# Kernel optimization log

Measured on AMD Instinct MI355X. Metric: run time of the kernel, lower is better.

## Reference

```python
import jax, jax.numpy as jnp
import numpy as np

N_NODES = 50000
N_EDGES = 800000
N_GLOBALS = 64
DX, DE, DU = 128, 32, 32
HID, OUT = 128, 128
EPS = 1e-5


def _mlp(x, W1, b1, W2, b2, g, b):
    # Linear -> ReLU -> Linear -> ReLU (activate_final) -> LayerNorm (normalize)
    h = jax.nn.relu(x @ W1 + b1)
    h = jax.nn.relu(h @ W2 + b2)
    mu = jnp.mean(h, axis=-1, keepdims=True)
    var = jnp.var(h, axis=-1, keepdims=True)
    return g * (h - mu) * jax.lax.rsqrt(var + EPS) + b


def _mlp_params(key, d_in):
    k1, k2 = jax.random.split(key)
    W1 = jax.random.normal(k1, (d_in, HID), jnp.float32) / np.sqrt(d_in)
    b1 = jnp.zeros((HID,), jnp.float32)
    W2 = jax.random.normal(k2, (HID, OUT), jnp.float32) / np.sqrt(HID)
    b2 = jnp.zeros((OUT,), jnp.float32)
    g = jnp.ones((OUT,), jnp.float32)
    b = jnp.zeros((OUT,), jnp.float32)
    return W1, b1, W2, b2, g, b


def setup_inputs() -> dict:
    key = jax.random.key(0)
    ks = jax.random.split(key, 8)
    x = jax.random.normal(ks[0], (N_NODES, DX), jnp.float32)
    e = jax.random.normal(ks[1], (N_EDGES, DE), jnp.float32)
    u = jax.random.normal(ks[2], (N_GLOBALS, DU), jnp.float32)
    edge_index = jax.random.randint(ks[3], (2, N_EDGES), 0, N_NODES, jnp.int64 if jax.config.jax_enable_x64 else jnp.int32)
    batch = jnp.sort(jax.random.randint(ks[4], (N_NODES,), 0, N_GLOBALS))
    # edge MLP in: e(32) + recv(128) + send(128) + u(32) = 320
    eW1, eb1, eW2, eb2, eg, ebt = _mlp_params(ks[5], DE + DX + DX + DU)
    # node MLP in: x(128) + edge_aggr(128) + u(32) = 288
    nW1, nb1, nW2, nb2, ng, nbt = _mlp_params(ks[6], DX + OUT + DU)
    # global MLP in: u(32) + node_aggr(128) + edge_aggr(128) = 288
    gW1, gb1, gW2, gb2, gg, gbt = _mlp_params(ks[7], DU + OUT + OUT)
    return dict(x=x, e=e, u=u, edge_index=edge_index, batch=batch,
                eW1=eW1, eb1=eb1, eW2=eW2, eb2=eb2, eg=eg, ebt=ebt,
                nW1=nW1, nb1=nb1, nW2=nW2, nb2=nb2, ng=ng, nbt=nbt,
                gW1=gW1, gb1=gb1, gW2=gW2, gb2=gb2, gg=gg, gbt=gbt)


def reference(x, e, u, edge_index, batch,
              eW1, eb1, eW2, eb2, eg, ebt,
              nW1, nb1, nW2, nb2, ng, nbt,
              gW1, gb1, gW2, gb2, gg, gbt):
    row, col = edge_index[0], edge_index[1]
    edge_batch = batch[row]  # graph id per edge

    # --- EdgeModel: concat(edge, receiver, sender, global->edges) -> MLP ---
    edge_in = jnp.concatenate([e, x[col], x[row], u[edge_batch]], axis=1)
    e2 = _mlp(edge_in, eW1, eb1, eW2, eb2, eg, ebt)  # [N_EDGES, OUT]

    # --- NodeModel: concat(node, edges->node via receiver, global->nodes) -> MLP ---
    edge_to_node = jax.ops.segment_sum(e2, col, num_segments=N_NODES)
    node_in = jnp.concatenate([x, edge_to_node, u[batch]], axis=1)
    x2 = _mlp(node_in, nW1, nb1, nW2, nb2, ng, nbt)  # [N_NODES, OUT]

    # --- GlobalModel: concat(global, nodes->global, edges->global) -> MLP ---
    node_to_glob = jax.ops.segment_sum(x2, batch, num_segments=N_GLOBALS)
    edge_to_glob = jax.ops.segment_sum(e2, edge_batch, num_segments=N_GLOBALS)
    glob_in = jnp.concatenate([u, node_to_glob, edge_to_glob], axis=1)
    u2 = _mlp(glob_in, gW1, gb1, gW2, gb2, gg, gbt)  # [N_GLOBALS, OUT]

    return x2, e2, u2
```

## Files before the change

### kernel.cpp

```cpp
#include <hip/hip_runtime.h>
#include <hip/hip_bf16.h>

typedef __attribute__((ext_vector_type(8))) short bf16x8;
typedef __attribute__((ext_vector_type(4))) float f32x4;

#define EPSV 1e-5f
#define NN 50000
#define NE 800000
#define NG 64
#define SEGB 1000
#define MFMA16(a, b, c) __builtin_amdgcn_mfma_f32_16x16x32_bf16(a, b, c, 0, 0, 0)

__device__ __forceinline__ unsigned short f2bf(float f) {
  union { float f; unsigned u; } v; v.f = f;
  unsigned r = v.u + 0x7FFFu + ((v.u >> 16) & 1u);
  return (unsigned short)(r >> 16);
}
__device__ __forceinline__ float bf2f(unsigned short h) {
  union { unsigned u; float f; } v; v.u = ((unsigned)h) << 16;
  return v.f;
}
__device__ __forceinline__ float bflo(unsigned u) {
  union { unsigned x; float f; } v; v.x = u << 16; return v.f;
}
__device__ __forceinline__ float bfhi(unsigned u) {
  union { unsigned x; float f; } v; v.x = u & 0xffff0000u; return v.f;
}


__global__ __launch_bounds__(256) void cvt_vec_kernel(
    const float* __restrict__ x, unsigned short* __restrict__ xb) {
  const int NX4 = (NN * 128) / 4;
  for (int idx = blockIdx.x * 256 + threadIdx.x; idx < NX4;
       idx += gridDim.x * 256) {
    float4 v = ((const float4*)x)[idx];
    ushort4 o;
    o.x = f2bf(v.x); o.y = f2bf(v.y); o.z = f2bf(v.z); o.w = f2bf(v.w);
    ((ushort4*)xb)[idx] = o;
  }
}

__global__ __launch_bounds__(256) void cvt_small_kernel(
    const float* __restrict__ u,
    const float* __restrict__ eW1, const float* __restrict__ eW2,
    const float* __restrict__ nW1, const float* __restrict__ nW2,
    unsigned short* __restrict__ ub,
    unsigned short* __restrict__ W1eT, unsigned short* __restrict__ WpqT,
    unsigned short* __restrict__ eW2T,
    unsigned short* __restrict__ nW1T, unsigned short* __restrict__ nW2T,
    float* __restrict__ Rg) {
  int i = blockIdx.x * 256 + threadIdx.x;
  const int R0 = NG * 32;
  const int R1 = R0 + 128 * 32;
  const int R2 = R1 + 256 * 128;
  const int R3 = R2 + 128 * 128;
  const int R4 = R3 + 128 * 320;
  const int R5 = R4 + 128 * 128;
  const int R6 = R5 + NG * 128;
  if (i < R0) {
    ub[i] = f2bf(u[i]);
  } else if (i < R1) {
    int j = i - R0; int n = j >> 5, k = j & 31;
    W1eT[j] = f2bf(eW1[k * 128 + n]);
  } else if (i < R2) {
    int j = i - R1; int n = j >> 7, k = j & 127;
    WpqT[j] = (n < 128) ? f2bf(eW1[(32 + k) * 128 + n])
                        : f2bf(eW1[(160 + k) * 128 + (n - 128)]);
  } else if (i < R3) {
    int j = i - R2; int n = j >> 7, k = j & 127;
    eW2T[j] = f2bf(eW2[k * 128 + n]);
  } else if (i < R4) {
    int j = i - R3; int n = j / 320, k = j % 320;
    nW1T[j] = (k < 288) ? f2bf(nW1[k * 128 + n]) : (unsigned short)0;
  } else if (i < R5) {
    int j = i - R4; int n = j >> 7, k = j & 127;
    nW2T[j] = f2bf(nW2[k * 128 + n]);
  } else if (i < R6) {
    int j = i - R5; int g = j >> 7, n = j & 127;
    float s = 0.f;
#pragma unroll
    for (int k = 0; k < 32; ++k) s += u[g * 32 + k] * eW1[(288 + k) * 128 + n];
    Rg[j] = s;
  }
}

__global__ __launch_bounds__(256, 2) void pq_kernel(
    const unsigned short* __restrict__ xb,
    const unsigned short* __restrict__ WpqT,
    unsigned short* __restrict__ PQ) {
  __shared__ __align__(16) unsigned short Asm[64][136];
  __shared__ __align__(16) unsigned short Bsm[256][72];
  const int tid = threadIdx.x;
  {
    const int r = tid >> 2, q = tid & 3;
    const int grow = blockIdx.x * 64 + r;
    const uint4 zero = {0u, 0u, 0u, 0u};
    if (grow < NN) {
      const uint4* xs = (const uint4*)(xb + (size_t)grow * 128 + q * 32);
#pragma unroll
      for (int k = 0; k < 4; ++k) *(uint4*)&Asm[r][q * 32 + k * 8] = xs[k];
    } else {
#pragma unroll
      for (int k = 0; k < 4; ++k) *(uint4*)&Asm[r][q * 32 + k * 8] = zero;
    }
  }
  const int w = tid >> 6, lane = tid & 63;
  const int l15 = lane & 15, lg = lane >> 4;
  f32x4 acc[16];
#pragma unroll
  for (int ni = 0; ni < 16; ++ni) acc[ni] = f32x4{0.f, 0.f, 0.f, 0.f};
  for (int kc = 0; kc < 2; ++kc) {
    {
      const uint4* src = (const uint4*)(WpqT + (size_t)tid * 128 + kc * 64);
#pragma unroll
      for (int k = 0; k < 8; ++k) *(uint4*)&Bsm[tid][k * 8] = src[k];
    }
    __syncthreads();
    bf16x8 a0 = *(bf16x8*)&Asm[w * 16 + l15][kc * 64 + lg * 8];
    bf16x8 a1 = *(bf16x8*)&Asm[w * 16 + l15][kc * 64 + 32 + lg * 8];
#pragma unroll
    for (int ni = 0; ni < 16; ++ni) {
      bf16x8 b0 = *(bf16x8*)&Bsm[ni * 16 + l15][lg * 8];
      bf16x8 b1 = *(bf16x8*)&Bsm[ni * 16 + l15][32 + lg * 8];
      acc[ni] = MFMA16(a0, b0, acc[ni]);
      acc[ni] = MFMA16(a1, b1, acc[ni]);
    }
    __syncthreads();
  }
  unsigned short (*Cl)[264] = (unsigned short(*)[264])&Bsm[0][0];
#pragma unroll
  for (int ni = 0; ni < 16; ++ni)
#pragma unroll
    for (int reg = 0; reg < 4; ++reg)
      Cl[w * 16 + lg * 4 + reg][l15 + ni * 16] = f2bf(acc[ni][reg]);
  __syncthreads();
  {
    const int r = tid >> 2, q = tid & 3;
    const int grow = blockIdx.x * 64 + r;
    if (grow < NN) {
#pragma unroll
      for (int k = 0; k < 8; ++k)
        *(uint4*)(PQ + (size_t)grow * 256 + q * 64 + k * 8) =
            *(uint4*)&Cl[r][q * 64 + k * 8];
    }
  }
}


__global__ __launch_bounds__(256) void pre_kernel(
    const int* __restrict__ rowIdx, const int* __restrict__ colIdx,
    int* __restrict__ cnt_r, int* __restrict__ cnt_s) {
  int i = blockIdx.x * 256 + threadIdx.x;
  if (i < NE) {
    atomicAdd(&cnt_r[colIdx[i]], 1);
    atomicAdd(&cnt_s[rowIdx[i]], 1);
  }
}

__global__ __launch_bounds__(1024) void scan2_kernel(
    const int* __restrict__ cnt_r, int* __restrict__ offs_r, int* __restrict__ cur_r,
    const int* __restrict__ cnt_s, int* __restrict__ offs_s, int* __restrict__ cur_s) {
  __shared__ int sums[1024];
  const int* cnt = blockIdx.x ? cnt_s : cnt_r;
  int* offs = blockIdx.x ? offs_s : offs_r;
  int* cur  = blockIdx.x ? cur_s : cur_r;
  const int t = threadIdx.x;
  const int base = t * 49;
  int s = 0;
  for (int j = 0; j < 49; ++j) {
    int idx = base + j;
    if (idx < NN) s += cnt[idx];
  }
  sums[t] = s;
  __syncthreads();
  for (int off = 1; off < 1024; off <<= 1) {
    int add = (t >= off) ? sums[t - off] : 0;
    __syncthreads();
    sums[t] += add;
    __syncthreads();
  }
  int run = (t == 0) ? 0 : sums[t - 1];
  for (int j = 0; j < 49; ++j) {
    int idx = base + j;
    if (idx < NN) {
      offs[idx] = run; cur[idx] = run;
      run += cnt[idx];
    }
  }
}

__global__ __launch_bounds__(256) void fill_both_kernel(
    const int* __restrict__ rowIdx, const int* __restrict__ colIdx,
    const int* __restrict__ batch,
    int* __restrict__ cur_r, int* __restrict__ cur_s,
    int* __restrict__ eidlist_r, int* __restrict__ eidlist_s,
    int* __restrict__ gs) {
  int i = blockIdx.x * 256 + threadIdx.x;
  if (i < NE) {
    const int c = colIdx[i];
    const int p = atomicAdd(&cur_r[c], 1);
    eidlist_r[p] = i;
    const int r = rowIdx[i];
    const int p2 = atomicAdd(&cur_s[r], 1);
    eidlist_s[p2] = i;
    gs[p2] = batch[r];
  }
}

__global__ __launch_bounds__(256, 3) void edge_kernel(
    const float* __restrict__ ef,
    const unsigned short* __restrict__ PQ,
    const float* __restrict__ Rg,
    const int* __restrict__ rowI, const int* __restrict__ colI,
    const int* __restrict__ batch,
    const unsigned short* __restrict__ W1eT,
    const unsigned short* __restrict__ W2T,
    const float* __restrict__ b1, const float* __restrict__ b2,
    const float* __restrict__ gam, const float* __restrict__ bet,
    float* __restrict__ outE, unsigned short* __restrict__ e2b) {
  __shared__ __align__(16) char U[27648];
  __shared__ __align__(16) unsigned short Hsm[64][136];
  __shared__ float cb1[128], cb2[128], cg[128], cbt[128];
  unsigned short (*B1e)[40] = (unsigned short(*)[40])U;
  unsigned short (*Ssm)[136] = (unsigned short(*)[136])(U + 10240);
  unsigned short (*Bsm)[72] = (unsigned short(*)[72])U;

  const int tid = threadIdx.x;
  const int base = blockIdx.x * 64;
  if (tid < 128) {
    cb1[tid] = b1[tid]; cb2[tid] = b2[tid];
    cg[tid] = gam[tid]; cbt[tid] = bet[tid];
    const uint4* s = (const uint4*)(W1eT + tid * 32);
#pragma unroll
    for (int k = 0; k < 4; ++k) *(uint4*)&B1e[tid][k * 8] = s[k];
  }

  {
    const int r = tid >> 2, q = tid & 3;
    const int grow = base + r;
    const int rcv = colI[grow];
    const int snd = rowI[grow];
    const int g = batch[snd];
    const unsigned short* pp = PQ + (size_t)rcv * 256 + q * 32;
    const unsigned short* qq = PQ + (size_t)snd * 256 + 128 + q * 32;
    const float* rr = Rg + g * 128 + q * 32;
#pragma unroll
    for (int k = 0; k < 8; ++k) {
      ushort4 pv = *(const ushort4*)(pp + k * 4);
      ushort4 qv = *(const ushort4*)(qq + k * 4);
      float4 rv = *(const float4*)(rr + k * 4);
      ushort4 o;
      o.x = f2bf(bf2f(pv.x) + bf2f(qv.x) + rv.x);
      o.y = f2bf(bf2f(pv.y) + bf2f(qv.y) + rv.y);
      o.z = f2bf(bf2f(pv.z) + bf2f(qv.z) + rv.z);
      o.w = f2bf(bf2f(pv.w) + bf2f(qv.w) + rv.w);
      *(ushort4*)&Ssm[r][q * 32 + k * 4] = o;
    }
  }
  __syncthreads();

  const int w = tid >> 6, lane = tid & 63;
  const int l15 = lane & 15, lg = lane >> 4;

  f32x4 acc[8];
#pragma unroll
  for (int ni = 0; ni < 8; ++ni) acc[ni] = f32x4{0.f, 0.f, 0.f, 0.f};
  {
    const int arow = base + w * 16 + l15;
    const float* ep = ef + (size_t)arow * 32 + lg * 8;
    float4 v0 = *(const float4*)ep;
    float4 v1 = *(const float4*)(ep + 4);
    bf16x8 a;
    a[0] = (short)f2bf(v0.x); a[1] = (short)f2bf(v0.y);
    a[2] = (short)f2bf(v0.z); a[3] = (short)f2bf(v0.w);
    a[4] = (short)f2bf(v1.x); a[5] = (short)f2bf(v1.y);
    a[6] = (short)f2bf(v1.z); a[7] = (short)f2bf(v1.w);
#pragma unroll
    for (int ni = 0; ni < 8; ++ni) {
      bf16x8 b0 = *(bf16x8*)&B1e[ni * 16 + l15][lg * 8];
      acc[ni] = MFMA16(a, b0, acc[ni]);
    }
  }

#pragma unroll
  for (int ni = 0; ni < 8; ++ni) {
    const int ncol = l15 + ni * 16;
    const float bias = cb1[ncol];
#pragma unroll
    for (int reg = 0; reg < 4; ++reg) {
      const int mrow = w * 16 + lg * 4 + reg;
      const float sv = bf2f(Ssm[mrow][ncol]);
      Hsm[mrow][ncol] = f2bf(fmaxf(acc[ni][reg] + sv + bias, 0.f));
    }
  }
  __syncthreads();

  f32x4 acc2[8];
#pragma unroll
  for (int ni = 0; ni < 8; ++ni) acc2[ni] = f32x4{0.f, 0.f, 0.f, 0.f};
  for (int kc = 0; kc < 2; ++kc) {
    {
      const int n = tid >> 1, half = tid & 1;
      const uint4* src = (const uint4*)(W2T + (size_t)n * 128 + kc * 64 + half * 32);
#pragma unroll
      for (int k = 0; k < 4; ++k)
        *(uint4*)&Bsm[n][half * 32 + k * 8] = src[k];
    }
    __syncthreads();
    bf16x8 a0 = *(bf16x8*)&Hsm[w * 16 + l15][kc * 64 + lg * 8];
    bf16x8 a1 = *(bf16x8*)&Hsm[w * 16 + l15][kc * 64 + 32 + lg * 8];
#pragma unroll
    for (int ni = 0; ni < 8; ++ni) {
      bf16x8 b0 = *(bf16x8*)&Bsm[ni * 16 + l15][lg * 8];
      bf16x8 b1 = *(bf16x8*)&Bsm[ni * 16 + l15][32 + lg * 8];
      acc2[ni] = MFMA16(a0, b0, acc2[ni]);
      acc2[ni] = MFMA16(a1, b1, acc2[ni]);
    }
    __syncthreads();
  }

  float hv[8][4];
  float sreg[4] = {0.f, 0.f, 0.f, 0.f}, ssreg[4] = {0.f, 0.f, 0.f, 0.f};
#pragma unroll
  for (int ni = 0; ni < 8; ++ni) {
    const int ncol = l15 + ni * 16;
    const float bias = cb2[ncol];
#pragma unroll
    for (int reg = 0; reg < 4; ++reg) {
      const float h = fmaxf(acc2[ni][reg] + bias, 0.f);
      hv[ni][reg] = h;
      sreg[reg] += h; ssreg[reg] += h * h;
    }
  }
#pragma unroll
  for (int reg = 0; reg < 4; ++reg) {
    float s = sreg[reg], ss = ssreg[reg];
#pragma unroll
    for (int off = 1; off < 16; off <<= 1) {
      s += __shfl_xor(s, off, 64);
      ss += __shfl_xor(ss, off, 64);
    }
    sreg[reg] = s; ssreg[reg] = ss;
  }
#pragma unroll
  for (int reg = 0; reg < 4; ++reg) {
    const int mrow = w * 16 + lg * 4 + reg;
    const int grow = base + mrow;
    const float mu = sreg[reg] * (1.f / 128.f);
    const float var = ssreg[reg] * (1.f / 128.f) - mu * mu;
    const float rstd = rsqrtf(var + EPSV);
#pragma unroll
    for (int ni = 0; ni < 8; ++ni) {
      const int ncol = l15 + ni * 16;
      const float y = cg[ncol] * (hv[ni][reg] - mu) * rstd + cbt[ncol];
      outE[(size_t)grow * 128 + ncol] = y;
      if (e2b) Hsm[mrow][ncol] = f2bf(y);
    }
  }
  if (e2b) {
    __syncthreads();
    const int r = tid >> 2, q = tid & 3;
#pragma unroll
    for (int k = 0; k < 4; ++k)
      *(uint4*)(e2b + (size_t)(base + r) * 128 + q * 32 + k * 8) =
          *(uint4*)&Hsm[r][q * 32 + k * 8];
  }
}

template <int BF>
__global__ __launch_bounds__(256, 2) void post_kernel(
    const float* __restrict__ outE, const unsigned short* __restrict__ e2b,
    const int* __restrict__ eidl_s, const int* __restrict__ gsA,
    float* __restrict__ e2g,
    const unsigned short* __restrict__ xb,
    const unsigned short* __restrict__ ub,
    const int* __restrict__ batch,
    const int* __restrict__ offs, const int* __restrict__ cnt,
    const int* __restrict__ eidlist,
    const unsigned short* __restrict__ W1T,
    const unsigned short* __restrict__ W2T,
    const float* __restrict__ b1, const float* __restrict__ b2,
    const float* __restrict__ gam, const float* __restrict__ bet,
    float* __restrict__ outX, float* __restrict__ n2g) {
  __shared__ __align__(16) char U[50176];
  __shared__ __align__(16) unsigned short Bsm[128][72];
  __shared__ float cb1[128], cb2[128], cg[128], cbt[128];

  const int tid = threadIdx.x;

  if (blockIdx.x < SEGB) {
    const int c4 = (tid & 31) * 4;
    const int sub = tid >> 5;
    const int start = blockIdx.x * 800;
    int gcur = gsA[start + sub];
    float4 acc = {0.f, 0.f, 0.f, 0.f};
    for (int it = 0; it < 25; ++it) {
      const int pbase = start + sub + it * 32;
      int eid[4], g[4];
#pragma unroll
      for (int j = 0; j < 4; ++j) {
        eid[j] = eidl_s[pbase + j * 8];
        g[j]   = gsA[pbase + j * 8];
      }
      float4 v[4];
      if (BF) {
#pragma unroll
        for (int j = 0; j < 4; ++j) {
          ushort4 h = *(const ushort4*)(e2b + (size_t)eid[j] * 128 + c4);
          v[j] = float4{bf2f(h.x), bf2f(h.y), bf2f(h.z), bf2f(h.w)};
        }
      } else {
#pragma unroll
        for (int j = 0; j < 4; ++j)
          v[j] = *(const float4*)(outE + (size_t)eid[j] * 128 + c4);
      }
#pragma unroll
      for (int j = 0; j < 4; ++j) {
        if (g[j] != gcur) {
          atomicAdd(&e2g[gcur * 128 + c4],     acc.x);
          atomicAdd(&e2g[gcur * 128 + c4 + 1], acc.y);
          atomicAdd(&e2g[gcur * 128 + c4 + 2], acc.z);
          atomicAdd(&e2g[gcur * 128 + c4 + 3], acc.w);
          gcur = g[j]; acc = float4{0.f, 0.f, 0.f, 0.f};
        }
        acc.x += v[j].x; acc.y += v[j].y; acc.z += v[j].z; acc.w += v[j].w;
      }
    }
    atomicAdd(&e2g[gcur * 128 + c4],     acc.x);
    atomicAdd(&e2g[gcur * 128 + c4 + 1], acc.y);
    atomicAdd(&e2g[gcur * 128 + c4 + 2], acc.z);
    atomicAdd(&e2g[gcur * 128 + c4 + 3], acc.w);
    return;
  }

  const int bx = blockIdx.x - SEGB;
  unsigned short (*Asm)[328] = (unsigned short(*)[328])U;
  unsigned short (*Hsm)[136] = (unsigned short(*)[136])U;
  float* bins = (float*)(U + 17408);

  if (tid < 128) {
    cb1[tid] = b1[tid]; cb2[tid] = b2[tid];
    cg[tid] = gam[tid]; cbt[tid] = bet[tid];
  }

  {
    const int r = tid >> 2, q = tid & 3;
    const int grow = bx * 64 + r;
    const bool valid = grow < NN;
    const uint4 zero = {0u, 0u, 0u, 0u};
    if (valid) {
      const uint4* xs = (const uint4*)(xb + (size_t)grow * 128 + q * 32);
#pragma unroll
      for (int k = 0; k < 4; ++k) *(uint4*)&Asm[r][q * 32 + k * 8] = xs[k];
    } else {
#pragma unroll
      for (int k = 0; k < 4; ++k) *(uint4*)&Asm[r][q * 32 + k * 8] = zero;
    }
    float4 a[8];
#pragma unroll
    for (int k = 0; k < 8; ++k) a[k] = float4{0.f, 0.f, 0.f, 0.f};
    if (valid) {
      const int start = offs[grow];
      const int deg = cnt[grow];
      int j = 0;
      for (; j + 2 <= deg; j += 2) {
        const int e0 = eidlist[start + j], e1 = eidlist[start + j + 1];
        if (BF) {
          const uint4* s0 = (const uint4*)(e2b + (size_t)e0 * 128 + q * 32);
          const uint4* s1 = (const uint4*)(e2b + (size_t)e1 * 128 + q * 32);
#pragma unroll
          for (int k = 0; k < 4; ++k) {
            uint4 v0 = s0[k], v1 = s1[k];
            a[2 * k].x     += bflo(v0.x) + bflo(v1.x);
            a[2 * k].y     += bfhi(v0.x) + bfhi(v1.x);
            a[2 * k].z     += bflo(v0.y) + bflo(v1.y);
            a[2 * k].w     += bfhi(v0.y) + bfhi(v1.y);
            a[2 * k + 1].x += bflo(v0.z) + bflo(v1.z);
            a[2 * k + 1].y += bfhi(v0.z) + bfhi(v1.z);
            a[2 * k + 1].z += bflo(v0.w) + bflo(v1.w);
            a[2 * k + 1].w += bfhi(v0.w) + bfhi(v1.w);
          }
        } else {
          const float4* s0 = (const float4*)(outE + (size_t)e0 * 128 + q * 32);
          const float4* s1 = (const float4*)(outE + (size_t)e1 * 128 + q * 32);
#pragma unroll
          for (int k = 0; k < 8; ++k) {
            float4 v0 = s0[k], v1 = s1[k];
            a[k].x += v0.x + v1.x; a[k].y += v0.y + v1.y;
            a[k].z += v0.z + v1.z; a[k].w += v0.w + v1.w;
          }
        }
      }
      if (j < deg) {
        const int e0 = eidlist[start + j];
        if (BF) {
          const uint4* s0 = (const uint4*)(e2b + (size_t)e0 * 128 + q * 32);
#pragma unroll
          for (int k = 0; k < 4; ++k) {
            uint4 v0 = s0[k];
            a[2 * k].x     += bflo(v0.x);
            a[2 * k].y     += bfhi(v0.x);
            a[2 * k].z     += bflo(v0.y);
            a[2 * k].w     += bfhi(v0.y);
            a[2 * k + 1].x += bflo(v0.z);
            a[2 * k + 1].y += bfhi(v0.z);
            a[2 * k + 1].z += bflo(v0.w);
            a[2 * k + 1].w += bfhi(v0.w);
          }
        } else {
          const float4* s0 = (const float4*)(outE + (size_t)e0 * 128 + q * 32);
#pragma unroll
          for (int k = 0; k < 8; ++k) {
            float4 v0 = s0[k];
            a[k].x += v0.x; a[k].y += v0.y; a[k].z += v0.z; a[k].w += v0.w;
          }
        }
      }
    }
#pragma unroll
    for (int k = 0; k < 8; ++k) {
      ushort4 o;
      o.x = f2bf(a[k].x); o.y = f2bf(a[k].y);
      o.z = f2bf(a[k].z); o.w = f2bf(a[k].w);
      *(ushort4*)&Asm[r][128 + q * 32 + k * 4] = o;
    }
    const int g = valid ? batch[grow] : 0;
    uint4 uv = valid ? *(const uint4*)(ub + g * 32 + q * 8) : zero;
    *(uint4*)&Asm[r][256 + q * 8] = uv;
    *(uint4*)&Asm[r][288 + q * 8] = zero;
  }

  const int w = tid >> 6;
  const int lane = tid & 63;
  const int l15 = lane & 15, lg = lane >> 4;

  f32x4 acc[8];
#pragma unroll
  for (int ni = 0; ni < 8; ++ni) acc[ni] = f32x4{0.f, 0.f, 0.f, 0.f};

  for (int kc = 0; kc < 5; ++kc) {
    {
      const int n = tid >> 1, half = tid & 1;
      const uint4* src = (const uint4*)(W1T + (size_t)n * 320 + kc * 64 + half * 32);
#pragma unroll
      for (int k = 0; k < 4; ++k)
        *(uint4*)&Bsm[n][half * 32 + k * 8] = src[k];
    }
    __syncthreads();
    bf16x8 a0 = *(bf16x8*)&Asm[w * 16 + l15][kc * 64 + lg * 8];
    bf16x8 a1 = *(bf16x8*)&Asm[w * 16 + l15][kc * 64 + 32 + lg * 8];
#pragma unroll
    for (int ni = 0; ni < 8; ++ni) {
      bf16x8 bb0 = *(bf16x8*)&Bsm[ni * 16 + l15][lg * 8];
      bf16x8 bb1 = *(bf16x8*)&Bsm[ni * 16 + l15][32 + lg * 8];
      acc[ni] = MFMA16(a0, bb0, acc[ni]);
      acc[ni] = MFMA16(a1, bb1, acc[ni]);
    }
    __syncthreads();
  }

#pragma unroll
  for (int ni = 0; ni < 8; ++ni) {
    const int ncol = l15 + ni * 16;
    const float bias = cb1[ncol];
#pragma unroll
    for (int reg = 0; reg < 4; ++reg) {
      const int mrow = w * 16 + lg * 4 + reg;
      Hsm[mrow][ncol] = f2bf(fmaxf(acc[ni][reg] + bias, 0.f));
    }
  }
  for (int i = tid; i < NG * 128; i += 256) bins[i] = 0.f;

  f32x4 acc2[8];
#pragma unroll
  for (int ni = 0; ni < 8; ++ni) acc2[ni] = f32x4{0.f, 0.f, 0.f, 0.f};
  for (int kc = 0; kc < 2; ++kc) {
    {
      const int n = tid >> 1, half = tid & 1;
      const uint4* src = (const uint4*)(W2T + (size_t)n * 128 + kc * 64 + half * 32);
#pragma unroll
      for (int k = 0; k < 4; ++k)
        *(uint4*)&Bsm[n][half * 32 + k * 8] = src[k];
    }
    __syncthreads();
    bf16x8 a0 = *(bf16x8*)&Hsm[w * 16 + l15][kc * 64 + lg * 8];
    bf16x8 a1 = *(bf16x8*)&Hsm[w * 16 + l15][kc * 64 + 32 + lg * 8];
#pragma unroll
    for (int ni = 0; ni < 8; ++ni) {
      bf16x8 bb0 = *(bf16x8*)&Bsm[ni * 16 + l15][lg * 8];
      bf16x8 bb1 = *(bf16x8*)&Bsm[ni * 16 + l15][32 + lg * 8];
      acc2[ni] = MFMA16(a0, bb0, acc2[ni]);
      acc2[ni] = MFMA16(a1, bb1, acc2[ni]);
    }
    __syncthreads();
  }

  float hv[8][4];
  float sreg[4] = {0.f, 0.f, 0.f, 0.f}, ssreg[4] = {0.f, 0.f, 0.f, 0.f};
#pragma unroll
  for (int ni = 0; ni < 8; ++ni) {
    const int ncol = l15 + ni * 16;
    const float bias = cb2[ncol];
#pragma unroll
    for (int reg = 0; reg < 4; ++reg) {
      const float h = fmaxf(acc2[ni][reg] + bias, 0.f);
      hv[ni][reg] = h;
      sreg[reg] += h; ssreg[reg] += h * h;
    }
  }
#pragma unroll
  for (int reg = 0; reg < 4; ++reg) {
    float s = sreg[reg], ss = ssreg[reg];
#pragma unroll
    for (int off = 1; off < 16; off <<= 1) {
      s += __shfl_xor(s, off, 64);
      ss += __shfl_xor(ss, off, 64);
    }
    sreg[reg] = s; ssreg[reg] = ss;
  }
#pragma unroll
  for (int reg = 0; reg < 4; ++reg) {
    const int mrow = w * 16 + lg * 4 + reg;
    const int grow = bx * 64 + mrow;
    if (grow >= NN) continue;
    const float mu = sreg[reg] * (1.f / 128.f);
    const float var = ssreg[reg] * (1.f / 128.f) - mu * mu;
    const float rstd = rsqrtf(var + EPSV);
    const int g = batch[grow];
#pragma unroll
    for (int ni = 0; ni < 8; ++ni) {
      const int ncol = l15 + ni * 16;
      const float y = cg[ncol] * (hv[ni][reg] - mu) * rstd + cbt[ncol];
      outX[(size_t)grow * 128 + ncol] = y;
      atomicAdd(&bins[g * 128 + ncol], y);
    }
  }
  __syncthreads();
  const int first = bx * 64;
  const int last = min(first + 63, NN - 1);
  const int gmin = batch[first], gmax = batch[last];
  const int cntf = (gmax - gmin + 1) * 128;
  for (int i = tid; i < cntf; i += 256)
    atomicAdd(&n2g[gmin * 128 + i], bins[gmin * 128 + i]);
}

__global__ __launch_bounds__(128) void glob_kernel(
    const float* __restrict__ u, const float* __restrict__ n2g,
    const float* __restrict__ e2g,
    const float* __restrict__ gW1, const float* __restrict__ gb1,
    const float* __restrict__ gW2, const float* __restrict__ gb2,
    const float* __restrict__ gg, const float* __restrict__ gbt,
    float* __restrict__ outU) {
  __shared__ float in[288];
  __shared__ float h1[128];
  __shared__ float red[4];
  const int g = blockIdx.x, t = threadIdx.x;
  if (t < 32) in[t] = u[g * 32 + t];
  in[32 + t] = n2g[g * 128 + t];
  in[160 + t] = e2g[g * 128 + t];
  __syncthreads();
  float a = gb1[t];
  for (int k = 0; k < 288; ++k) a += in[k] * gW1[k * 128 + t];
  h1[t] = fmaxf(a, 0.f);
  __syncthreads();
  float h = gb2[t];
  for (int k = 0; k < 128; ++k) h += h1[k] * gW2[k * 128 + t];
  h = fmaxf(h, 0.f);
  float s = h, ss = h * h;
  for (int off = 1; off < 64; off <<= 1) {
    s += __shfl_xor(s, off, 64);
    ss += __shfl_xor(ss, off, 64);
  }
  if ((t & 63) == 0) { red[(t >> 6) * 2] = s; red[(t >> 6) * 2 + 1] = ss; }
  __syncthreads();
  const float S = red[0] + red[2], SS = red[1] + red[3];
  const float mu = S * (1.f / 128.f);
  const float var = SS * (1.f / 128.f) - mu * mu;
  const float rstd = rsqrtf(var + EPSV);
  outU[g * 128 + t] = gg[t] * (h - mu) * rstd + gbt[t];
}

extern "C" void kernel_launch(void* const* d_in, const int* in_sizes, int n_in,
                              void* d_out, int out_size, void* d_ws,
                              size_t ws_size, hipStream_t stream) {
  const float* x   = (const float*)d_in[0];
  const float* e   = (const float*)d_in[1];
  const float* u   = (const float*)d_in[2];
  const int* eidx  = (const int*)d_in[3];
  const int* batch = (const int*)d_in[4];
  const float* eW1 = (const float*)d_in[5];
  const float* eb1 = (const float*)d_in[6];
  const float* eW2 = (const float*)d_in[7];
  const float* eb2 = (const float*)d_in[8];
  const float* eg  = (const float*)d_in[9];
  const float* ebt = (const float*)d_in[10];
  const float* nW1 = (const float*)d_in[11];
  const float* nb1 = (const float*)d_in[12];
  const float* nW2 = (const float*)d_in[13];
  const float* nb2 = (const float*)d_in[14];
  const float* ng  = (const float*)d_in[15];
  const float* nbt = (const float*)d_in[16];
  const float* gW1 = (const float*)d_in[17];
  const float* gb1 = (const float*)d_in[18];
  const float* gW2 = (const float*)d_in[19];
  const float* gb2 = (const float*)d_in[20];
  const float* gg  = (const float*)d_in[21];
  const float* gbt = (const float*)d_in[22];

  char* ws = (char*)d_ws;
  float* e2g           = (float*)(ws + 0);
  float* n2g           = (float*)(ws + 32768);
  int*   cnt_r         = (int*)  (ws + 65536);
  int*   cnt_s         = (int*)  (ws + 265536);
  int*   offs_r        = (int*)  (ws + 465536);
  int*   cur_r         = (int*)  (ws + 665536);
  int*   offs_s        = (int*)  (ws + 865536);
  int*   cur_s         = (int*)  (ws + 1065536);
  int*   eidlist_r     = (int*)  (ws + 1265536);
  int*   eidlist_s     = (int*)  (ws + 4465536);
  int*   gs            = (int*)  (ws + 7665536);
  unsigned short* xb   = (unsigned short*)(ws + 10865536);
  unsigned short* ub   = (unsigned short*)(ws + 23665536);
  unsigned short* W1eT = (unsigned short*)(ws + 23669632);
  unsigned short* WpqT = (unsigned short*)(ws + 23677824);
  unsigned short* eW2T = (unsigned short*)(ws + 23743360);
  unsigned short* nW1T = (unsigned short*)(ws + 23776128);
  unsigned short* nW2T = (unsigned short*)(ws + 23858048);
  unsigned short* PQ   = (unsigned short*)(ws + 23890816);
  float* Rg            = (float*)(ws + 49490816);
  unsigned short* e2b  = (unsigned short*)(ws + 49523584);
  const bool useB = ws_size >= (size_t)49523584 + 204800000;

  hipMemsetAsync(ws, 0, 465536, stream);

  cvt_vec_kernel<<<1024, 256, 0, stream>>>(x, xb);
  cvt_small_kernel<<<472, 256, 0, stream>>>(u, eW1, eW2, nW1, nW2, ub, W1eT,
                                            WpqT, eW2T, nW1T, nW2T, Rg);
  pq_kernel<<<(NN + 63) / 64, 256, 0, stream>>>(xb, WpqT, PQ);

  float* outX = (float*)d_out;
  float* outE = outX + (size_t)NN * 128;
  float* outU = outE + (size_t)NE * 128;

  const int* rowI = eidx;
  const int* colI = eidx + NE;

  pre_kernel<<<(NE + 255) / 256, 256, 0, stream>>>(rowI, colI, cnt_r, cnt_s);
  scan2_kernel<<<2, 1024, 0, stream>>>(cnt_r, offs_r, cur_r,
                                       cnt_s, offs_s, cur_s);
  fill_both_kernel<<<(NE + 255) / 256, 256, 0, stream>>>(
      rowI, colI, batch, cur_r, cur_s, eidlist_r, eidlist_s, gs);

  edge_kernel<<<NE / 64, 256, 0, stream>>>(e, PQ, Rg, rowI, colI, batch,
                                           W1eT, eW2T, eb1, eb2, eg, ebt,
                                           outE, useB ? e2b : nullptr);
  if (useB) {
    post_kernel<1><<<SEGB + (NN + 63) / 64, 256, 0, stream>>>(
        outE, e2b, eidlist_s, gs, e2g,
        xb, ub, batch, offs_r, cnt_r, eidlist_r,
        nW1T, nW2T, nb1, nb2, ng, nbt, outX, n2g);
  } else {
    post_kernel<0><<<SEGB + (NN + 63) / 64, 256, 0, stream>>>(
        outE, e2b, eidlist_s, gs, e2g,
        xb, ub, batch, offs_r, cnt_r, eidlist_r,
        nW1T, nW2T, nb1, nb2, ng, nbt, outX, n2g);
  }
  glob_kernel<<<NG, 128, 0, stream>>>(u, n2g, e2g, gW1, gb1, gW2, gb2, gg, gbt,
                                      outU);
}
```

Before: 827.5 us.

## Shrink edge kernel LDS footprint to raise occupancy to five blocks

Cuts the edge kernel's shared memory: the gather result and the hidden activations now share one buffer, updated in place, and the W2 staging buffer shrinks to 32-wide K chunks that reuse the W1 buffer. The launch bound goes from 3 to 5 blocks per CU. The gather loop also moves to 16-byte loads with packed bf16 stores. In exchange there are four K-chunks with more barriers instead of two, and a tighter register budget that may spill.

```diff
diff --git a/kernel.cpp b/kernel.cpp
--- a/kernel.cpp
+++ b/kernel.cpp
@@ -207,7 +207,7 @@
   }
 }
 
-__global__ __launch_bounds__(256, 3) void edge_kernel(
+__global__ __launch_bounds__(256, 5) void edge_kernel(
     const float* __restrict__ ef,
     const unsigned short* __restrict__ PQ,
     const float* __restrict__ Rg,
@@ -218,12 +218,9 @@
     const float* __restrict__ b1, const float* __restrict__ b2,
     const float* __restrict__ gam, const float* __restrict__ bet,
     float* __restrict__ outE, unsigned short* __restrict__ e2b) {
-  __shared__ __align__(16) char U[27648];
-  __shared__ __align__(16) unsigned short Hsm[64][136];
+  __shared__ __align__(16) unsigned short UB[128][40];
+  __shared__ __align__(16) unsigned short SH[64][136];
   __shared__ float cb1[128], cb2[128], cg[128], cbt[128];
-  unsigned short (*B1e)[40] = (unsigned short(*)[40])U;
-  unsigned short (*Ssm)[136] = (unsigned short(*)[136])(U + 10240);
-  unsigned short (*Bsm)[72] = (unsigned short(*)[72])U;
 
   const int tid = threadIdx.x;
   const int base = blockIdx.x * 64;
@@ -232,7 +229,7 @@
     cg[tid] = gam[tid]; cbt[tid] = bet[tid];
     const uint4* s = (const uint4*)(W1eT + tid * 32);
 #pragma unroll
-    for (int k = 0; k < 4; ++k) *(uint4*)&B1e[tid][k * 8] = s[k];
+    for (int k = 0; k < 4; ++k) *(uint4*)&UB[tid][k * 8] = s[k];
   }
 
   {
@@ -241,20 +238,22 @@
     const int rcv = colI[grow];
     const int snd = rowI[grow];
     const int g = batch[snd];
-    const unsigned short* pp = PQ + (size_t)rcv * 256 + q * 32;
-    const unsigned short* qq = PQ + (size_t)snd * 256 + 128 + q * 32;
-    const float* rr = Rg + g * 128 + q * 32;
-#pragma unroll
-    for (int k = 0; k < 8; ++k) {
-      ushort4 pv = *(const ushort4*)(pp + k * 4);
-      ushort4 qv = *(const ushort4*)(qq + k * 4);
-      float4 rv = *(const float4*)(rr + k * 4);
-      ushort4 o;
-      o.x = f2bf(bf2f(pv.x) + bf2f(qv.x) + rv.x);
-      o.y = f2bf(bf2f(pv.y) + bf2f(qv.y) + rv.y);
-      o.z = f2bf(bf2f(pv.z) + bf2f(qv.z) + rv.z);
-      o.w = f2bf(bf2f(pv.w) + bf2f(qv.w) + rv.w);
-      *(ushort4*)&Ssm[r][q * 32 + k * 4] = o;
+    const uint4* pp = (const uint4*)(PQ + (size_t)rcv * 256 + q * 32);
+    const uint4* qq = (const uint4*)(PQ + (size_t)snd * 256 + 128 + q * 32);
+    const float4* rr = (const float4*)(Rg + g * 128 + q * 32);
+#pragma unroll
+    for (int k = 0; k < 4; ++k) {
+      uint4 pv = pp[k], qv = qq[k];
+      float4 r0 = rr[2 * k], r1 = rr[2 * k + 1];
+      unsigned o0 = (unsigned)f2bf(bflo(pv.x) + bflo(qv.x) + r0.x)
+                  | ((unsigned)f2bf(bfhi(pv.x) + bfhi(qv.x) + r0.y) << 16);
+      unsigned o1 = (unsigned)f2bf(bflo(pv.y) + bflo(qv.y) + r0.z)
+                  | ((unsigned)f2bf(bfhi(pv.y) + bfhi(qv.y) + r0.w) << 16);
+      unsigned o2 = (unsigned)f2bf(bflo(pv.z) + bflo(qv.z) + r1.x)
+                  | ((unsigned)f2bf(bfhi(pv.z) + bfhi(qv.z) + r1.y) << 16);
+      unsigned o3 = (unsigned)f2bf(bflo(pv.w) + bflo(qv.w) + r1.z)
+                  | ((unsigned)f2bf(bfhi(pv.w) + bfhi(qv.w) + r1.w) << 16);
+      *(uint4*)&SH[r][q * 32 + k * 8] = uint4{o0, o1, o2, o3};
     }
   }
   __syncthreads();
@@ -277,7 +276,7 @@
     a[6] = (short)f2bf(v1.z); a[7] = (short)f2bf(v1.w);
 #pragma unroll
     for (int ni = 0; ni < 8; ++ni) {
-      bf16x8 b0 = *(bf16x8*)&B1e[ni * 16 + l15][lg * 8];
+      bf16x8 b0 = *(bf16x8*)&UB[ni * 16 + l15][lg * 8];
       acc[ni] = MFMA16(a, b0, acc[ni]);
     }
   }
@@ -289,8 +288,8 @@
 #pragma unroll
     for (int reg = 0; reg < 4; ++reg) {
       const int mrow = w * 16 + lg * 4 + reg;
-      const float sv = bf2f(Ssm[mrow][ncol]);
-      Hsm[mrow][ncol] = f2bf(fmaxf(acc[ni][reg] + sv + bias, 0.f));
+      const float sv = bf2f(SH[mrow][ncol]);
+      SH[mrow][ncol] = f2bf(fmaxf(acc[ni][reg] + sv + bias, 0.f));
     }
   }
   __syncthreads();
@@ -298,23 +297,19 @@
   f32x4 acc2[8];
 #pragma unroll
   for (int ni = 0; ni < 8; ++ni) acc2[ni] = f32x4{0.f, 0.f, 0.f, 0.f};
-  for (int kc = 0; kc < 2; ++kc) {
+  for (int kc = 0; kc < 4; ++kc) {
     {
       const int n = tid >> 1, half = tid & 1;
-      const uint4* src = (const uint4*)(W2T + (size_t)n * 128 + kc * 64 + half * 32);
-#pragma unroll
-      for (int k = 0; k < 4; ++k)
-        *(uint4*)&Bsm[n][half * 32 + k * 8] = src[k];
-    }
-    __syncthreads();
-    bf16x8 a0 = *(bf16x8*)&Hsm[w * 16 + l15][kc * 64 + lg * 8];
-    bf16x8 a1 = *(bf16x8*)&Hsm[w * 16 + l15][kc * 64 + 32 + lg * 8];
+      const uint4* src = (const uint4*)(W2T + (size_t)n * 128 + kc * 32 + half * 16);
+      *(uint4*)&UB[n][half * 16] = src[0];
+      *(uint4*)&UB[n][half * 16 + 8] = src[1];
+    }
+    __syncthreads();
+    bf16x8 a0 = *(bf16x8*)&SH[w * 16 + l15][kc * 32 + lg * 8];
 #pragma unroll
     for (int ni = 0; ni < 8; ++ni) {
-      bf16x8 b0 = *(bf16x8*)&Bsm[ni * 16 + l15][lg * 8];
-      bf16x8 b1 = *(bf16x8*)&Bsm[ni * 16 + l15][32 + lg * 8];
-      acc2[ni] = MFMA16(a0, b0, acc2[ni]);
-      acc2[ni] = MFMA16(a1, b1, acc2[ni]);
+      bf16x8 bb = *(bf16x8*)&UB[ni * 16 + l15][lg * 8];
+      acc2[ni] = MFMA16(a0, bb, acc2[ni]);
     }
     __syncthreads();
   }
@@ -354,7 +349,7 @@
       const int ncol = l15 + ni * 16;
       const float y = cg[ncol] * (hv[ni][reg] - mu) * rstd + cbt[ncol];
       outE[(size_t)grow * 128 + ncol] = y;
-      if (e2b) Hsm[mrow][ncol] = f2bf(y);
+      if (e2b) SH[mrow][ncol] = f2bf(y);
     }
   }
   if (e2b) {
@@ -363,7 +358,7 @@
 #pragma unroll
     for (int k = 0; k < 4; ++k)
       *(uint4*)(e2b + (size_t)(base + r) * 128 + q * 32 + k * 8) =
-          *(uint4*)&Hsm[r][q * 32 + k * 8];
+          *(uint4*)&SH[r][q * 32 + k * 8];
   }
 }
 
```

After: 840.8 us. Within noise of the previous version (+1.6%).

## Store bf16 edge outputs in receiver-sorted order to make node aggregation contiguous

Applied to the files above, without the earlier changes.

The edge kernel now writes its bf16 copy of e2 at the edge's position in the receiver-sorted CSR order (posr), so the node-side aggregation reads contiguous rows instead of gathering through eidlist. A new segmap kernel remaps the sender-sorted list to these new positions for the edge-to-global reduction. The edge-kernel gather of PQ/Rg is also widened to 16-byte loads. In exchange the edge kernel's bf16 stores are scattered, and there is an extra kernel plus more workspace use. The fp32 fallback path is unchanged.

```diff
diff --git a/kernel.cpp b/kernel.cpp
--- a/kernel.cpp
+++ b/kernel.cpp
@@ -193,12 +193,13 @@
     const int* __restrict__ rowIdx, const int* __restrict__ colIdx,
     const int* __restrict__ batch,
     int* __restrict__ cur_r, int* __restrict__ cur_s,
-    int* __restrict__ eidlist_r, int* __restrict__ eidlist_s,
-    int* __restrict__ gs) {
+    int* __restrict__ posr, int* __restrict__ eidlist_r,
+    int* __restrict__ eidlist_s, int* __restrict__ gs) {
   int i = blockIdx.x * 256 + threadIdx.x;
   if (i < NE) {
     const int c = colIdx[i];
     const int p = atomicAdd(&cur_r[c], 1);
+    posr[i] = p;
     eidlist_r[p] = i;
     const int r = rowIdx[i];
     const int p2 = atomicAdd(&cur_s[r], 1);
@@ -207,12 +208,19 @@
   }
 }
 
+__global__ __launch_bounds__(256) void segmap_kernel(
+    const int* __restrict__ eidl_s, const int* __restrict__ posr,
+    int* __restrict__ segidx) {
+  int i = blockIdx.x * 256 + threadIdx.x;
+  if (i < NE) segidx[i] = posr[eidl_s[i]];
+}
+
 __global__ __launch_bounds__(256, 3) void edge_kernel(
     const float* __restrict__ ef,
     const unsigned short* __restrict__ PQ,
     const float* __restrict__ Rg,
     const int* __restrict__ rowI, const int* __restrict__ colI,
-    const int* __restrict__ batch,
+    const int* __restrict__ batch, const int* __restrict__ posr,
     const unsigned short* __restrict__ W1eT,
     const unsigned short* __restrict__ W2T,
     const float* __restrict__ b1, const float* __restrict__ b2,
@@ -241,20 +249,22 @@
     const int rcv = colI[grow];
     const int snd = rowI[grow];
     const int g = batch[snd];
-    const unsigned short* pp = PQ + (size_t)rcv * 256 + q * 32;
-    const unsigned short* qq = PQ + (size_t)snd * 256 + 128 + q * 32;
-    const float* rr = Rg + g * 128 + q * 32;
-#pragma unroll
-    for (int k = 0; k < 8; ++k) {
-      ushort4 pv = *(const ushort4*)(pp + k * 4);
-      ushort4 qv = *(const ushort4*)(qq + k * 4);
-      float4 rv = *(const float4*)(rr + k * 4);
-      ushort4 o;
-      o.x = f2bf(bf2f(pv.x) + bf2f(qv.x) + rv.x);
-      o.y = f2bf(bf2f(pv.y) + bf2f(qv.y) + rv.y);
-      o.z = f2bf(bf2f(pv.z) + bf2f(qv.z) + rv.z);
-      o.w = f2bf(bf2f(pv.w) + bf2f(qv.w) + rv.w);
-      *(ushort4*)&Ssm[r][q * 32 + k * 4] = o;
+    const uint4* pp = (const uint4*)(PQ + (size_t)rcv * 256 + q * 32);
+    const uint4* qq = (const uint4*)(PQ + (size_t)snd * 256 + 128 + q * 32);
+    const float4* rr = (const float4*)(Rg + g * 128 + q * 32);
+#pragma unroll
+    for (int k = 0; k < 4; ++k) {
+      uint4 pv = pp[k], qv = qq[k];
+      float4 r0 = rr[2 * k], r1 = rr[2 * k + 1];
+      unsigned o0 = (unsigned)f2bf(bflo(pv.x) + bflo(qv.x) + r0.x)
+                  | ((unsigned)f2bf(bfhi(pv.x) + bfhi(qv.x) + r0.y) << 16);
+      unsigned o1 = (unsigned)f2bf(bflo(pv.y) + bflo(qv.y) + r0.z)
+                  | ((unsigned)f2bf(bfhi(pv.y) + bfhi(qv.y) + r0.w) << 16);
+      unsigned o2 = (unsigned)f2bf(bflo(pv.z) + bflo(qv.z) + r1.x)
+                  | ((unsigned)f2bf(bfhi(pv.z) + bfhi(qv.z) + r1.y) << 16);
+      unsigned o3 = (unsigned)f2bf(bflo(pv.w) + bflo(qv.w) + r1.z)
+                  | ((unsigned)f2bf(bfhi(pv.w) + bfhi(qv.w) + r1.w) << 16);
+      *(uint4*)&Ssm[r][q * 32 + k * 8] = uint4{o0, o1, o2, o3};
     }
   }
   __syncthreads();
@@ -360,9 +370,10 @@
   if (e2b) {
     __syncthreads();
     const int r = tid >> 2, q = tid & 3;
+    const int drow = posr[base + r];
 #pragma unroll
     for (int k = 0; k < 4; ++k)
-      *(uint4*)(e2b + (size_t)(base + r) * 128 + q * 32 + k * 8) =
+      *(uint4*)(e2b + (size_t)drow * 128 + q * 32 + k * 8) =
           *(uint4*)&Hsm[r][q * 32 + k * 8];
   }
 }
@@ -370,7 +381,7 @@
 template <int BF>
 __global__ __launch_bounds__(256, 2) void post_kernel(
     const float* __restrict__ outE, const unsigned short* __restrict__ e2b,
-    const int* __restrict__ eidl_s, const int* __restrict__ gsA,
+    const int* __restrict__ segA, const int* __restrict__ gsA,
     float* __restrict__ e2g,
     const unsigned short* __restrict__ xb,
     const unsigned short* __restrict__ ub,
@@ -399,7 +410,7 @@
       int eid[4], g[4];
 #pragma unroll
       for (int j = 0; j < 4; ++j) {
-        eid[j] = eidl_s[pbase + j * 8];
+        eid[j] = segA[pbase + j * 8];
         g[j]   = gsA[pbase + j * 8];
       }
       float4 v[4];
@@ -464,10 +475,9 @@
       const int deg = cnt[grow];
       int j = 0;
       for (; j + 2 <= deg; j += 2) {
-        const int e0 = eidlist[start + j], e1 = eidlist[start + j + 1];
         if (BF) {
-          const uint4* s0 = (const uint4*)(e2b + (size_t)e0 * 128 + q * 32);
-          const uint4* s1 = (const uint4*)(e2b + (size_t)e1 * 128 + q * 32);
+          const uint4* s0 = (const uint4*)(e2b + (size_t)(start + j) * 128 + q * 32);
+          const uint4* s1 = (const uint4*)(e2b + (size_t)(start + j + 1) * 128 + q * 32);
 #pragma unroll
           for (int k = 0; k < 4; ++k) {
             uint4 v0 = s0[k], v1 = s1[k];
@@ -481,6 +491,7 @@
             a[2 * k + 1].w += bfhi(v0.w) + bfhi(v1.w);
           }
         } else {
+          const int e0 = eidlist[start + j], e1 = eidlist[start + j + 1];
           const float4* s0 = (const float4*)(outE + (size_t)e0 * 128 + q * 32);
           const float4* s1 = (const float4*)(outE + (size_t)e1 * 128 + q * 32);
 #pragma unroll
@@ -492,9 +503,8 @@
         }
       }
       if (j < deg) {
-        const int e0 = eidlist[start + j];
         if (BF) {
-          const uint4* s0 = (const uint4*)(e2b + (size_t)e0 * 128 + q * 32);
+          const uint4* s0 = (const uint4*)(e2b + (size_t)(start + j) * 128 + q * 32);
 #pragma unroll
           for (int k = 0; k < 4; ++k) {
             uint4 v0 = s0[k];
@@ -508,6 +518,7 @@
             a[2 * k + 1].w += bfhi(v0.w);
           }
         } else {
+          const int e0 = eidlist[start + j];
           const float4* s0 = (const float4*)(outE + (size_t)e0 * 128 + q * 32);
 #pragma unroll
           for (int k = 0; k < 8; ++k) {
@@ -719,17 +730,19 @@
   int*   eidlist_r     = (int*)  (ws + 1265536);
   int*   eidlist_s     = (int*)  (ws + 4465536);
   int*   gs            = (int*)  (ws + 7665536);
-  unsigned short* xb   = (unsigned short*)(ws + 10865536);
-  unsigned short* ub   = (unsigned short*)(ws + 23665536);
-  unsigned short* W1eT = (unsigned short*)(ws + 23669632);
-  unsigned short* WpqT = (unsigned short*)(ws + 23677824);
-  unsigned short* eW2T = (unsigned short*)(ws + 23743360);
-  unsigned short* nW1T = (unsigned short*)(ws + 23776128);
-  unsigned short* nW2T = (unsigned short*)(ws + 23858048);
-  unsigned short* PQ   = (unsigned short*)(ws + 23890816);
-  float* Rg            = (float*)(ws + 49490816);
-  unsigned short* e2b  = (unsigned short*)(ws + 49523584);
-  const bool useB = ws_size >= (size_t)49523584 + 204800000;
+  int*   posr          = (int*)  (ws + 10865536);
+  int*   segidx        = (int*)  (ws + 14065536);
+  unsigned short* xb   = (unsigned short*)(ws + 17265536);
+  unsigned short* ub   = (unsigned short*)(ws + 30065536);
+  unsigned short* W1eT = (unsigned short*)(ws + 30069632);
+  unsigned short* WpqT = (unsigned short*)(ws + 30077824);
+  unsigned short* eW2T = (unsigned short*)(ws + 30143360);
+  unsigned short* nW1T = (unsigned short*)(ws + 30176128);
+  unsigned short* nW2T = (unsigned short*)(ws + 30258048);
+  unsigned short* PQ   = (unsigned short*)(ws + 30290816);
+  float* Rg            = (float*)(ws + 55890816);
+  unsigned short* e2b  = (unsigned short*)(ws + 55923584);
+  const bool useB = ws_size >= (size_t)55923584 + 204800000;
 
   hipMemsetAsync(ws, 0, 465536, stream);
 
@@ -749,14 +762,15 @@
   scan2_kernel<<<2, 1024, 0, stream>>>(cnt_r, offs_r, cur_r,
                                        cnt_s, offs_s, cur_s);
   fill_both_kernel<<<(NE + 255) / 256, 256, 0, stream>>>(
-      rowI, colI, batch, cur_r, cur_s, eidlist_r, eidlist_s, gs);
-
-  edge_kernel<<<NE / 64, 256, 0, stream>>>(e, PQ, Rg, rowI, colI, batch,
+      rowI, colI, batch, cur_r, cur_s, posr, eidlist_r, eidlist_s, gs);
+  segmap_kernel<<<(NE + 255) / 256, 256, 0, stream>>>(eidlist_s, posr, segidx);
+
+  edge_kernel<<<NE / 64, 256, 0, stream>>>(e, PQ, Rg, rowI, colI, batch, posr,
                                            W1eT, eW2T, eb1, eb2, eg, ebt,
                                            outE, useB ? e2b : nullptr);
   if (useB) {
     post_kernel<1><<<SEGB + (NN + 63) / 64, 256, 0, stream>>>(
-        outE, e2b, eidlist_s, gs, e2g,
+        outE, e2b, segidx, gs, e2g,
         xb, ub, batch, offs_r, cnt_r, eidlist_r,
         nW1T, nW2T, nb1, nb2, ng, nbt, outX, n2g);
   } else {
```

New measurement: 826.5 us. No clear change (-0.1%).
